# Performance work log

Hardware: AMD Instinct MI355X
Metric: run time of the kernel (lower is better)

Reference implementation:

```python
import jax, jax.numpy as jnp
import numpy as np

EMB = 1024
HEADS = 16
HEAD = EMB // HEADS
B, S = 4, 1024


def setup_inputs() -> dict:
    key = jax.random.key(0)
    ks = jax.random.split(key, 8)
    glorot = lambda k, shp: jax.random.normal(k, shp, jnp.float32) * np.sqrt(2.0 / (shp[-2] + shp[-1]))
    return {
        "inputs_for_keys": jax.random.normal(ks[0], (B, S, EMB), jnp.float32),
        "inputs_for_values": jax.random.normal(ks[1], (B, S, EMB), jnp.float32),
        "inputs_for_queries": jax.random.normal(ks[2], (B, S, EMB), jnp.float32),
        "Wk": glorot(ks[3], (HEADS, EMB, HEAD)),
        "Wv": glorot(ks[4], (HEADS, EMB, HEAD)),
        "Wq": glorot(ks[5], (HEADS, EMB, HEAD)),
        "Wo": glorot(ks[6], (EMB, EMB)),
        "bo": jnp.zeros((EMB,), jnp.float32),
    }


def reference(inputs_for_keys, inputs_for_values, inputs_for_queries, Wk, Wv, Wq, Wo, bo):
    # Batched equivalent of the per-head loop: project all heads at once.
    K = jnp.einsum("bse,hed->bhsd", inputs_for_keys, Wk)
    V = jnp.einsum("bse,hed->bhsd", inputs_for_values, Wv)
    Q = jnp.einsum("bse,hed->bhsd", inputs_for_queries, Wq)
    s_keys = K.shape[2]
    s_q = Q.shape[2]
    # causal mask: -inf strictly above diagonal (original: np.triu(ones*-inf, k=1))
    mask = jnp.where(jnp.triu(jnp.ones((s_q, s_keys), bool), k=1), -jnp.inf, 0.0).astype(jnp.float32)
    logits = jnp.einsum("bhqd,bhkd->bhqk", Q, K)
    # FAITHFUL quirk: original divides (logits + mask) by sqrt(window_size_keys)
    scores = jax.nn.softmax((logits + mask) / np.sqrt(s_keys), axis=-1)
    ctx = jnp.einsum("bhqk,bhkd->bhqd", scores, V)  # [B,H,Sq,Dh]
    # concat heads along last dim (head order matches loop order)
    concat = ctx.transpose(0, 2, 1, 3).reshape(ctx.shape[0], s_q, -1)  # [B,Sq,E]
    return jax.nn.relu(concat @ Wo + bo)
```

## Files before the change

### kernel.cpp

```cpp
#include <hip/hip_runtime.h>
#include <hip/hip_bf16.h>

typedef unsigned short u16;
typedef unsigned int   u32;
typedef __attribute__((ext_vector_type(4))) float f32x4;
typedef __attribute__((ext_vector_type(8))) short bf16x8;
typedef __attribute__((ext_vector_type(4))) short bf16x4;

#define EMB   1024
#define SEQ   1024
#define HEADS 16
#define DH    64
#define BATCH 4
#define BH    64
#define BS    4096
#define LDP   72
#define NEG_BIG (-1.0e30f)

__device__ __forceinline__ float b2f(u16 u){ return __uint_as_float(((u32)u) << 16); }
__device__ __forceinline__ u16 f2b(float f){
    u32 u = __float_as_uint(f);
    u32 r = u + 0x7fffu + ((u >> 16) & 1u);
    return (u16)(r >> 16);
}
__device__ __forceinline__ void zero4(f32x4& v){ v[0]=0.f; v[1]=0.f; v[2]=0.f; v[3]=0.f; }
__device__ __forceinline__ ushort4 pk4(float a, float b, float c, float d){
    ushort4 p; p.x = f2b(a); p.y = f2b(b); p.z = f2b(c); p.w = f2b(d); return p;
}

__device__ __forceinline__ void gld_lds16(const void* g, void* l){
    __builtin_amdgcn_global_load_lds(
        (const __attribute__((address_space(1))) u32*)g,
        (__attribute__((address_space(3))) u32*)l, 16, 0, 0);
}

__device__ __forceinline__ u16* tptr(u16* base, int row, int col ){
    const int phys = ((col >> 3) ^ (row & 7));
    return base + row * 64 + (phys << 3);
}
__device__ __forceinline__ const u16* tptrc(const u16* base, int row, int col ){
    const int phys = ((col >> 3) ^ (row & 7));
    return base + row * 64 + (phys << 3);
}
__device__ __forceinline__ const u16* tptr8c(const u16* base, int row, int col ){
    const int chunk = ((col >> 3) ^ (row & 7));
    return base + row * 64 + (chunk << 3) + (col & 7);
}

__device__ __forceinline__ void dot2_f32(const float* __restrict__ x,
                                         const float* __restrict__ w, const int ws,
                                         float& a0, float& a1)
{
    float s0 = 0.f, s1 = 0.f;
    for (int e = 0; e < EMB; e += 4) {
        const float4 xv = *(const float4*)(x + e);
        const float2 w0 = *(const float2*)(w + (size_t)(e + 0) * ws);
        const float2 w1 = *(const float2*)(w + (size_t)(e + 1) * ws);
        const float2 w2 = *(const float2*)(w + (size_t)(e + 2) * ws);
        const float2 w3 = *(const float2*)(w + (size_t)(e + 3) * ws);
        s0 += xv.x * w0.x; s1 += xv.x * w0.y;
        s0 += xv.y * w1.x; s1 += xv.y * w1.y;
        s0 += xv.z * w2.x; s1 += xv.z * w2.y;
        s0 += xv.w * w3.x; s1 += xv.w * w3.y;
    }
    a0 = s0; a1 = s1;
}


__global__ __launch_bounds__(256) void convert_x(
    const float* __restrict__ Xk, const float* __restrict__ Xv, const float* __restrict__ Xq,
    u16* __restrict__ XB)
{
    const int which = blockIdx.y;
    const float* __restrict__ src = (which == 0) ? Xk : (which == 1) ? Xv : Xq;
    const size_t off = (size_t)blockIdx.x * 1024 + threadIdx.x * 4;
    const float4 v = *(const float4*)(src + off);
    *(ushort4*)(XB + (size_t)which * 4194304 + off) = pk4(v.x, v.y, v.z, v.w);
}

__global__ __launch_bounds__(256) void transpose_w(
    const float* __restrict__ Wk, const float* __restrict__ Wv, const float* __restrict__ Wq,
    const float* __restrict__ Wo, u16* __restrict__ WT, u16* __restrict__ WoT)
{
    __shared__ u16 T[64][LDP];
    const int which = blockIdx.y;
    const int bx = blockIdx.x, t = threadIdx.x;

    if (which < 3) {
        const float* __restrict__ W = (which == 0) ? Wk : (which == 1) ? Wv : Wq;
        const int h = bx >> 4, e0 = (bx & 15) * 64;
        #pragma unroll
        for (int i = 0; i < 16; ++i) {
            const int idx = i * 256 + t;
            const int e = idx >> 6, d = idx & 63;
            T[d][e] = f2b(W[(size_t)h * (EMB * DH) + (size_t)(e0 + e) * DH + d]);
        }
        __syncthreads();
        u16* dstb = WT + (size_t)which * (EMB * EMB / 16) * 16;
        #pragma unroll
        for (int i = 0; i < 2; ++i) {
            const int idx = i * 256 + t;
            const int d = idx >> 3, e8 = (idx & 7) * 8;
            *(bf16x8*)(dstb + (size_t)(h * 64 + d) * EMB + e0 + e8) = *(const bf16x8*)&T[d][e8];
        }
    } else {
        const int j0 = (bx >> 4) * 64, e0 = (bx & 15) * 64;
        #pragma unroll
        for (int i = 0; i < 16; ++i) {
            const int idx = i * 256 + t;
            const int e = idx >> 6, d = idx & 63;
            T[d][e] = f2b(Wo[(size_t)(e0 + e) * EMB + j0 + d]);
        }
        __syncthreads();
        #pragma unroll
        for (int i = 0; i < 2; ++i) {
            const int idx = i * 256 + t;
            const int d = idx >> 3, e8 = (idx & 7) * 8;
            *(bf16x8*)(WoT + (size_t)(j0 + d) * EMB + e0 + e8) = *(const bf16x8*)&T[d][e8];
        }
    }
}

template<int MODE>
__global__ __launch_bounds__(256) void gemm128(
    const u16* __restrict__ XB, const u16* __restrict__ WT,
    u16* __restrict__ Qw, u16* __restrict__ Kw, u16* __restrict__ Vt,
    const float* __restrict__ bo, float* __restrict__ OUT)
{
    __shared__ u16 As[2][128 * 64];
    __shared__ u16 Bs[2][128 * 64];

    const int t = threadIdx.x;
    const int wave = t >> 6, lane = t & 63;
    const int quad = lane >> 4, l16 = lane & 15;
    const int wrow = wave >> 1, wcol = wave & 1;
    const int m0 = blockIdx.x * 128;
    const int n0 = blockIdx.y * 128;
    const int which = blockIdx.z;

    const u16* __restrict__ Ag = (MODE == 0) ? XB + (size_t)which * 4194304 : XB;
    const u16* __restrict__ Bg = (MODE == 0) ? WT + (size_t)which * 1048576 : WT;

    f32x4 acc[4][4];
    #pragma unroll
    for (int mi = 0; mi < 4; ++mi)
        #pragma unroll
        for (int ni = 0; ni < 4; ++ni) zero4(acc[mi][ni]);

    auto STAGE = [&](int kk, int buf){
        #pragma unroll
        for (int j = 0; j < 4; ++j) {
            const int cg = wave * 4 + j;
            const int c  = cg * 64 + lane;
            const int row = c >> 3;
            const int col = ((c ^ row) & 7) << 3;
            gld_lds16(Ag + (size_t)(m0 + row) * EMB + kk + col, &As[buf][cg * 512]);
            gld_lds16(Bg + (size_t)(n0 + row) * EMB + kk + col, &Bs[buf][cg * 512]);
        }
    };
    auto COMPUTE = [&](const u16* Ac, const u16* Bc){
        #pragma unroll
        for (int kb = 0; kb < 2; ++kb) {
            bf16x8 af[4], bf[4];
            #pragma unroll
            for (int mi = 0; mi < 4; ++mi)
                af[mi] = *(const bf16x8*)tptrc(Ac, wrow * 64 + mi * 16 + l16, kb * 32 + quad * 8);
            #pragma unroll
            for (int ni = 0; ni < 4; ++ni)
                bf[ni] = *(const bf16x8*)tptrc(Bc, wcol * 64 + ni * 16 + l16, kb * 32 + quad * 8);
            #pragma unroll
            for (int mi = 0; mi < 4; ++mi)
                #pragma unroll
                for (int ni = 0; ni < 4; ++ni)
                    acc[mi][ni] = __builtin_amdgcn_mfma_f32_16x16x32_bf16(af[mi], bf[ni], acc[mi][ni], 0, 0, 0);
        }
    };

    STAGE(0, 0);
    STAGE(64, 1);

    #pragma unroll
    for (int k = 0; k < 16; ++k) {
        if (k < 15) { asm volatile("s_waitcnt vmcnt(8)" ::: "memory"); }
        else        { asm volatile("s_waitcnt vmcnt(0)" ::: "memory"); }
        __builtin_amdgcn_sched_barrier(0);
        __builtin_amdgcn_s_barrier();
        __builtin_amdgcn_sched_barrier(0);

        COMPUTE(&As[k & 1][0], &Bs[k & 1][0]);

        asm volatile("s_waitcnt lgkmcnt(0)" ::: "memory");
        __builtin_amdgcn_sched_barrier(0);
        __builtin_amdgcn_s_barrier();
        __builtin_amdgcn_sched_barrier(0);

        if (k < 14) STAGE((k + 2) * 64, k & 1);
    }

    #pragma unroll
    for (int mi = 0; mi < 4; ++mi) {
        const int r = m0 + wrow * 64 + mi * 16 + quad * 4;
        #pragma unroll
        for (int ni = 0; ni < 4; ++ni) {
            const int j = n0 + wcol * 64 + ni * 16 + l16;
            if (MODE == 1) {
                const float bias = bo[j];
                #pragma unroll
                for (int reg = 0; reg < 4; ++reg) {
                    float v = acc[mi][ni][reg] + bias;
                    if (v < 0.f) v = 0.f;
                    OUT[(size_t)(r + reg) * EMB + j] = v;
                }
            } else {
                const int h = j >> 6, d = j & 63;
                const int b = r >> 10, s = r & (SEQ - 1);
                const int bh = b * HEADS + h;
                if (which == 1) {
                    *(ushort4*)(Vt + ((size_t)bh * DH + d) * SEQ + s) =
                        pk4(acc[mi][ni][0], acc[mi][ni][1], acc[mi][ni][2], acc[mi][ni][3]);
                } else {
                    u16* dst = (which == 0) ? Kw : Qw;
                    const float qsc = (which == 2) ? 0.03125f : 1.0f;
                    #pragma unroll
                    for (int reg = 0; reg < 4; ++reg)
                        dst[((size_t)bh * SEQ + s + reg) * DH + d] = f2b(acc[mi][ni][reg] * qsc);
                }
            }
        }
    }
}

__global__ __launch_bounds__(256) void attn_flash2(
    const u16* __restrict__ Qg, const u16* __restrict__ Kg, const u16* __restrict__ Vg,
    u16* __restrict__ CTXb)
{
    __shared__ u16 Ks[2][64 * 64];
    __shared__ u16 Vs[2][64 * 64];

    const int t = threadIdx.x;
    const int wave = t >> 6, lane = t & 63;
    const int quad = lane >> 4, l16 = lane & 15;
    const int bh = blockIdx.y;
    const int qt = (blockIdx.x + (blockIdx.y >> 2)) & 15;
    const int b = bh >> 4, h = bh & (HEADS - 1);
    const int q0 = qt * 64;

    const u16* __restrict__ Kbase = Kg + (size_t)bh * SEQ * DH;
    const u16* __restrict__ Vbase = Vg + (size_t)bh * DH * SEQ;

    bf16x8 qf[2];
    {
        const u16* qrow = Qg + ((size_t)bh * SEQ + q0 + wave * 16 + l16) * DH;
        qf[0] = *(const bf16x8*)(qrow + quad * 8);
        qf[1] = *(const bf16x8*)(qrow + 32 + quad * 8);
    }

    #pragma unroll
    for (int i = 0; i < 2; ++i) {
        const int c = i * 256 + t;
        const int row = c >> 3, col8 = (c & 7) * 8;
        const bf16x8 kv = *(const bf16x8*)(Kbase + (size_t)row * DH + col8);
        const bf16x8 vv = *(const bf16x8*)(Vbase + (size_t)row * SEQ + col8);
        *(bf16x8*)tptr(&Ks[0][0], row, col8) = kv;
        *(bf16x8*)tptr(&Vs[0][0], row, col8) = vv;
    }

    float m = NEG_BIG, l = 0.f;
    f32x4 oacc[4];
    #pragma unroll
    for (int nd = 0; nd < 4; ++nd) zero4(oacc[nd]);

    __syncthreads();

    const int qin = wave * 16 + l16;
    int cur = 0;
    for (int c = 0; c <= qt; ++c) {
        const int kn = ((c < qt) ? c + 1 : qt) * 64;
        bf16x8 kpre[2], vpre[2];
        #pragma unroll
        for (int i = 0; i < 2; ++i) {
            const int cc = i * 256 + t;
            const int row = cc >> 3, col8 = (cc & 7) * 8;
            kpre[i] = *(const bf16x8*)(Kbase + (size_t)(kn + row) * DH + col8);
            vpre[i] = *(const bf16x8*)(Vbase + (size_t)row * SEQ + kn + col8);
        }

        const u16* Kc = &Ks[cur][0];
        const u16* Vc = &Vs[cur][0];

        f32x4 sacc[4];
        #pragma unroll
        for (int ni = 0; ni < 4; ++ni) zero4(sacc[ni]);
        __builtin_amdgcn_s_setprio(1);
        #pragma unroll
        for (int kb = 0; kb < 2; ++kb) {
            #pragma unroll
            for (int ni = 0; ni < 4; ++ni) {
                const bf16x8 kf = *(const bf16x8*)tptrc(Kc, ni * 16 + l16, kb * 32 + quad * 8);
                sacc[ni] = __builtin_amdgcn_mfma_f32_16x16x32_bf16(kf, qf[kb], sacc[ni], 0, 0, 0);
            }
        }
        __builtin_amdgcn_s_setprio(0);

        const bool diag = (c == qt);
        float mx = m;
        #pragma unroll
        for (int ni = 0; ni < 4; ++ni) {
            #pragma unroll
            for (int reg = 0; reg < 4; ++reg) {
                float s = sacc[ni][reg];
                if (diag && (ni * 16 + quad * 4 + reg > qin)) s = NEG_BIG;
                sacc[ni][reg] = s;
                mx = fmaxf(mx, s);
            }
        }
        mx = fmaxf(mx, __shfl_xor(mx, 16));
        mx = fmaxf(mx, __shfl_xor(mx, 32));
        const float alpha = __expf(m - mx);
        m = mx;
        float rs = 0.f;
        bf16x4 pa[4];
        #pragma unroll
        for (int ni = 0; ni < 4; ++ni) {
            const float p0 = __expf(sacc[ni][0] - mx);
            const float p1 = __expf(sacc[ni][1] - mx);
            const float p2 = __expf(sacc[ni][2] - mx);
            const float p3 = __expf(sacc[ni][3] - mx);
            rs += (p0 + p1) + (p2 + p3);
            bf16x4 pk;
            pk[0] = (short)f2b(p0); pk[1] = (short)f2b(p1);
            pk[2] = (short)f2b(p2); pk[3] = (short)f2b(p3);
            pa[ni] = pk;
        }
        rs += __shfl_xor(rs, 16);
        rs += __shfl_xor(rs, 32);
        l = l * alpha + rs;

        #pragma unroll
        for (int reg = 0; reg < 4; ++reg) {
            const float ar = __shfl(alpha, quad * 4 + reg);
            #pragma unroll
            for (int nd = 0; nd < 4; ++nd) oacc[nd][reg] *= ar;
        }

        __builtin_amdgcn_s_setprio(1);
        #pragma unroll
        for (int ks = 0; ks < 4; ++ks) {
            #pragma unroll
            for (int nd = 0; nd < 4; ++nd) {
                const bf16x4 vf = *(const bf16x4*)tptr8c(Vc, nd * 16 + l16, ks * 16 + quad * 4);
                oacc[nd] = __builtin_amdgcn_mfma_f32_16x16x16bf16_1k(pa[ks], vf, oacc[nd], 0, 0, 0);
            }
        }
        __builtin_amdgcn_s_setprio(0);

        const int nxt = cur ^ 1;
        #pragma unroll
        for (int i = 0; i < 2; ++i) {
            const int cc = i * 256 + t;
            const int row = cc >> 3, col8 = (cc & 7) * 8;
            *(bf16x8*)tptr(&Ks[nxt][0], row, col8) = kpre[i];
            *(bf16x8*)tptr(&Vs[nxt][0], row, col8) = vpre[i];
        }
        __syncthreads();
        cur = nxt;
    }

    #pragma unroll
    for (int reg = 0; reg < 4; ++reg) {
        const float il = 1.f / __shfl(l, quad * 4 + reg);
        const int q = q0 + wave * 16 + quad * 4 + reg;
        #pragma unroll
        for (int nd = 0; nd < 4; ++nd) {
            const int d = nd * 16 + l16;
            CTXb[(size_t)(b * SEQ + q) * EMB + h * DH + d] = f2b(oacc[nd][reg] * il);
        }
    }
}


__global__ __launch_bounds__(256) void qkv_proj_mfma(
    const float* __restrict__ Xk, const float* __restrict__ Xv, const float* __restrict__ Xq,
    const float* __restrict__ Wk, const float* __restrict__ Wv, const float* __restrict__ Wq,
    u16* __restrict__ Kw, u16* __restrict__ Vw, u16* __restrict__ Qw)
{
    __shared__ u16 As[128][LDP];
    __shared__ u16 Bs[64][LDP];

    const int which = blockIdx.z;
    const float* __restrict__ X = (which == 0) ? Xk : (which == 1) ? Xv : Xq;
    const float* __restrict__ W = (which == 0) ? Wk : (which == 1) ? Wv : Wq;

    const int h    = blockIdx.y;
    const int m0   = blockIdx.x * 128;
    const int t    = threadIdx.x;
    const int wave = t >> 6, lane = t & 63;
    const int quad = lane >> 4, l16 = lane & 15;

    f32x4 acc[2][4];
    #pragma unroll
    for (int mi = 0; mi < 2; ++mi)
        #pragma unroll
        for (int ni = 0; ni < 4; ++ni) zero4(acc[mi][ni]);

    const size_t wbase = (size_t)h * EMB * DH;
    for (int k0 = 0; k0 < EMB; k0 += 64) {
        #pragma unroll
        for (int i = 0; i < 8; ++i) {
            const int idx = i * 256 + t;
            const int r = idx >> 4, c4 = (idx & 15) * 4;
            const float4 v = *(const float4*)(X + (size_t)(m0 + r) * EMB + k0 + c4);
            *(ushort4*)&As[r][c4] = pk4(v.x, v.y, v.z, v.w);
        }
        #pragma unroll
        for (int i = 0; i < 4; ++i) {
            const int d  = t & 63;
            const int e0 = (t >> 6) * 4 + i * 16;
            const float v0 = W[wbase + (size_t)(k0 + e0 + 0) * DH + d];
            const float v1 = W[wbase + (size_t)(k0 + e0 + 1) * DH + d];
            const float v2 = W[wbase + (size_t)(k0 + e0 + 2) * DH + d];
            const float v3 = W[wbase + (size_t)(k0 + e0 + 3) * DH + d];
            *(ushort4*)&Bs[d][e0] = pk4(v0, v1, v2, v3);
        }
        __syncthreads();

        #pragma unroll
        for (int kb = 0; kb < 2; ++kb) {
            bf16x8 bfr[4];
            #pragma unroll
            for (int ni = 0; ni < 4; ++ni)
                bfr[ni] = *(const bf16x8*)&Bs[ni * 16 + l16][kb * 32 + quad * 8];
            #pragma unroll
            for (int mi = 0; mi < 2; ++mi) {
                const bf16x8 af = *(const bf16x8*)&As[wave * 32 + mi * 16 + l16][kb * 32 + quad * 8];
                #pragma unroll
                for (int ni = 0; ni < 4; ++ni)
                    acc[mi][ni] = __builtin_amdgcn_mfma_f32_16x16x32_bf16(af, bfr[ni], acc[mi][ni], 0, 0, 0);
            }
        }
        __syncthreads();
    }

    const int b  = m0 >> 10;
    const int bh = b * HEADS + h;
    u16* __restrict__ RowDst = (which == 0) ? Kw : Qw;
    #pragma unroll
    for (int mi = 0; mi < 2; ++mi) {
        const int s_base = (m0 & (SEQ - 1)) + wave * 32 + mi * 16 + quad * 4;
        #pragma unroll
        for (int ni = 0; ni < 4; ++ni) {
            const int d = ni * 16 + l16;
            if (which != 1) {
                #pragma unroll
                for (int reg = 0; reg < 4; ++reg)
                    RowDst[((size_t)bh * SEQ + s_base + reg) * DH + d] = f2b(acc[mi][ni][reg]);
            } else {
                *(ushort4*)(Vw + ((size_t)bh * DH + d) * SEQ + s_base) =
                    pk4(acc[mi][ni][0], acc[mi][ni][1], acc[mi][ni][2], acc[mi][ni][3]);
            }
        }
    }
}

template<bool QWS, bool TOWS>
__global__ __launch_bounds__(256) void attn_flash(
    const float* __restrict__ Xq, const float* __restrict__ Wq,
    const u16* __restrict__ Qg, const u16* __restrict__ Kg, const u16* __restrict__ Vg,
    u16* __restrict__ CTXb, float* __restrict__ CTXf)
{
    __shared__ u16 Qs[64][LDP];
    union KVU {
        struct { u16 Ks[64][LDP]; u16 Vt[64][LDP]; } kv;
        struct { u16 Xs[64][LDP]; u16 WT[64][LDP]; } pr;
    };
    __shared__ KVU uu;
    __shared__ u16 Ps[64][LDP];

    const int t    = threadIdx.x;
    const int wave = t >> 6, lane = t & 63;
    const int quad = lane >> 4, l16 = lane & 15;
    const int qt = blockIdx.x, bh = blockIdx.y;
    const int b  = bh >> 4, h = bh & (HEADS - 1);
    const int q0 = qt * 64;

    if (QWS) {
        #pragma unroll
        for (int i = 0; i < 4; ++i) {
            const int idx = i * 256 + t;
            const int r = idx >> 4, c4 = (idx & 15) * 4;
            *(ushort4*)&Qs[r][c4] = *(const ushort4*)(Qg + ((size_t)bh * SEQ + q0 + r) * DH + c4);
        }
    } else {
        f32x4 qacc[4];
        #pragma unroll
        for (int ni = 0; ni < 4; ++ni) zero4(qacc[ni]);
        const size_t wbase = (size_t)h * EMB * DH;
        for (int k0 = 0; k0 < EMB; k0 += 64) {
            #pragma unroll
            for (int i = 0; i < 4; ++i) {
                const int idx = i * 256 + t;
                const int r = idx >> 4, c4 = (idx & 15) * 4;
                const float4 v = *(const float4*)(Xq + (size_t)(b * SEQ + q0 + r) * EMB + k0 + c4);
                *(ushort4*)&uu.pr.Xs[r][c4] = pk4(v.x, v.y, v.z, v.w);
            }
            #pragma unroll
            for (int i = 0; i < 4; ++i) {
                const int d  = t & 63;
                const int e0 = (t >> 6) * 4 + i * 16;
                const float v0 = Wq[wbase + (size_t)(k0 + e0 + 0) * DH + d];
                const float v1 = Wq[wbase + (size_t)(k0 + e0 + 1) * DH + d];
                const float v2 = Wq[wbase + (size_t)(k0 + e0 + 2) * DH + d];
                const float v3 = Wq[wbase + (size_t)(k0 + e0 + 3) * DH + d];
                *(ushort4*)&uu.pr.WT[d][e0] = pk4(v0, v1, v2, v3);
            }
            __syncthreads();
            #pragma unroll
            for (int kb = 0; kb < 2; ++kb) {
                const bf16x8 af = *(const bf16x8*)&uu.pr.Xs[wave * 16 + l16][kb * 32 + quad * 8];
                #pragma unroll
                for (int ni = 0; ni < 4; ++ni) {
                    const bf16x8 bf = *(const bf16x8*)&uu.pr.WT[ni * 16 + l16][kb * 32 + quad * 8];
                    qacc[ni] = __builtin_amdgcn_mfma_f32_16x16x32_bf16(af, bf, qacc[ni], 0, 0, 0);
                }
            }
            __syncthreads();
        }
        #pragma unroll
        for (int ni = 0; ni < 4; ++ni)
            #pragma unroll
            for (int reg = 0; reg < 4; ++reg)
                Qs[wave * 16 + quad * 4 + reg][ni * 16 + l16] = f2b(qacc[ni][reg]);
    }

    float m[4], l[4];
    #pragma unroll
    for (int reg = 0; reg < 4; ++reg) { m[reg] = NEG_BIG; l[reg] = 0.f; }
    f32x4 oacc[4];
    #pragma unroll
    for (int ni = 0; ni < 4; ++ni) zero4(oacc[ni]);
    __syncthreads();

    for (int c = 0; c <= qt; ++c) {
        const int k0 = c * 64;

        #pragma unroll
        for (int i = 0; i < 4; ++i) {
            const int idx = i * 256 + t;
            const int r = idx >> 4, c4 = (idx & 15) * 4;
            *(ushort4*)&uu.kv.Ks[r][c4] = *(const ushort4*)(Kg + ((size_t)bh * SEQ + k0 + r) * DH + c4);
        }
        #pragma unroll
        for (int i = 0; i < 4; ++i) {
            const int idx = i * 256 + t;
            const int r = idx >> 4, c4 = (idx & 15) * 4;
            *(ushort4*)&uu.kv.Vt[r][c4] = *(const ushort4*)(Vg + ((size_t)bh * DH + r) * SEQ + k0 + c4);
        }
        __syncthreads();

        f32x4 sacc[4];
        #pragma unroll
        for (int ni = 0; ni < 4; ++ni) zero4(sacc[ni]);
        #pragma unroll
        for (int kb = 0; kb < 2; ++kb) {
            const bf16x8 af = *(const bf16x8*)&Qs[wave * 16 + l16][kb * 32 + quad * 8];
            #pragma unroll
            for (int ni = 0; ni < 4; ++ni) {
                const bf16x8 bf = *(const bf16x8*)&uu.kv.Ks[ni * 16 + l16][kb * 32 + quad * 8];
                sacc[ni] = __builtin_amdgcn_mfma_f32_16x16x32_bf16(af, bf, sacc[ni], 0, 0, 0);
            }
        }

        const bool diag = (c == qt);
        #pragma unroll
        for (int reg = 0; reg < 4; ++reg) {
            const int rloc = quad * 4 + reg;
            float sv[4];
            #pragma unroll
            for (int ni = 0; ni < 4; ++ni) {
                float s = sacc[ni][reg] * 0.03125f;
                if (diag && (ni * 16 + l16 > wave * 16 + rloc)) s = NEG_BIG;
                sv[ni] = s;
            }
            float mx = fmaxf(fmaxf(sv[0], sv[1]), fmaxf(sv[2], sv[3]));
            mx = fmaxf(mx, m[reg]);
            #pragma unroll
            for (int off = 1; off < 16; off <<= 1) mx = fmaxf(mx, __shfl_xor(mx, off));
            const float alpha = __expf(m[reg] - mx);
            float rs = 0.f;
            #pragma unroll
            for (int ni = 0; ni < 4; ++ni) {
                const float p = __expf(sv[ni] - mx);
                Ps[wave * 16 + rloc][ni * 16 + l16] = f2b(p);
                rs += p;
            }
            #pragma unroll
            for (int off = 1; off < 16; off <<= 1) rs += __shfl_xor(rs, off);
            l[reg] = l[reg] * alpha + rs;
            m[reg] = mx;
            #pragma unroll
            for (int ni = 0; ni < 4; ++ni) oacc[ni][reg] *= alpha;
        }
        __syncthreads();

        #pragma unroll
        for (int kb = 0; kb < 2; ++kb) {
            const bf16x8 af = *(const bf16x8*)&Ps[wave * 16 + l16][kb * 32 + quad * 8];
            #pragma unroll
            for (int ni = 0; ni < 4; ++ni) {
                const bf16x8 bf = *(const bf16x8*)&uu.kv.Vt[ni * 16 + l16][kb * 32 + quad * 8];
                oacc[ni] = __builtin_amdgcn_mfma_f32_16x16x32_bf16(af, bf, oacc[ni], 0, 0, 0);
            }
        }
        __syncthreads();
    }

    float il[4];
    #pragma unroll
    for (int reg = 0; reg < 4; ++reg) il[reg] = 1.f / l[reg];
    #pragma unroll
    for (int ni = 0; ni < 4; ++ni) {
        const int d = ni * 16 + l16;
        #pragma unroll
        for (int reg = 0; reg < 4; ++reg) {
            const int q = wave * 16 + quad * 4 + reg;
            const float val = oacc[ni][reg] * il[reg];
            const size_t off = ((size_t)(b * SEQ + q0 + q)) * EMB + h * DH + d;
            if (TOWS) CTXb[off] = f2b(val);
            else      CTXf[off] = val;
        }
    }
}

__global__ __launch_bounds__(256) void out_proj_mfma(
    const u16* __restrict__ CTXb, const float* __restrict__ Wo,
    const float* __restrict__ bo, float* __restrict__ OUT)
{
    __shared__ u16 As[128][LDP];
    __shared__ u16 Bs[64][LDP];

    const int m0 = blockIdx.x * 128;
    const int n0 = blockIdx.y * 64;
    const int t = threadIdx.x;
    const int wave = t >> 6, lane = t & 63;
    const int quad = lane >> 4, l16 = lane & 15;

    f32x4 acc[2][4];
    #pragma unroll
    for (int mi = 0; mi < 2; ++mi)
        #pragma unroll
        for (int ni = 0; ni < 4; ++ni) zero4(acc[mi][ni]);

    for (int k0 = 0; k0 < EMB; k0 += 64) {
        #pragma unroll
        for (int i = 0; i < 8; ++i) {
            const int idx = i * 256 + t;
            const int r = idx >> 4, c4 = (idx & 15) * 4;
            *(ushort4*)&As[r][c4] = *(const ushort4*)(CTXb + (size_t)(m0 + r) * EMB + k0 + c4);
        }
        #pragma unroll
        for (int i = 0; i < 4; ++i) {
            const int d  = t & 63;
            const int e0 = (t >> 6) * 4 + i * 16;
            const float v0 = Wo[(size_t)(k0 + e0 + 0) * EMB + n0 + d];
            const float v1 = Wo[(size_t)(k0 + e0 + 1) * EMB + n0 + d];
            const float v2 = Wo[(size_t)(k0 + e0 + 2) * EMB + n0 + d];
            const float v3 = Wo[(size_t)(k0 + e0 + 3) * EMB + n0 + d];
            *(ushort4*)&Bs[d][e0] = pk4(v0, v1, v2, v3);
        }
        __syncthreads();
        #pragma unroll
        for (int kb = 0; kb < 2; ++kb) {
            bf16x8 bfr[4];
            #pragma unroll
            for (int ni = 0; ni < 4; ++ni)
                bfr[ni] = *(const bf16x8*)&Bs[ni * 16 + l16][kb * 32 + quad * 8];
            #pragma unroll
            for (int mi = 0; mi < 2; ++mi) {
                const bf16x8 af = *(const bf16x8*)&As[wave * 32 + mi * 16 + l16][kb * 32 + quad * 8];
                #pragma unroll
                for (int ni = 0; ni < 4; ++ni)
                    acc[mi][ni] = __builtin_amdgcn_mfma_f32_16x16x32_bf16(af, bfr[ni], acc[mi][ni], 0, 0, 0);
            }
        }
        __syncthreads();
    }

    #pragma unroll
    for (int mi = 0; mi < 2; ++mi) {
        const int row = m0 + wave * 32 + mi * 16 + quad * 4;
        #pragma unroll
        for (int ni = 0; ni < 4; ++ni) {
            const int col = n0 + ni * 16 + l16;
            const float bias = bo[col];
            #pragma unroll
            for (int reg = 0; reg < 4; ++reg) {
                float v = acc[mi][ni][reg] + bias;
                if (v < 0.f) v = 0.f;
                OUT[(size_t)(row + reg) * EMB + col] = v;
            }
        }
    }
}

__global__ __launch_bounds__(256) void out_proj_inplace(
    float* __restrict__ OUT, const float* __restrict__ Wo, const float* __restrict__ bo)
{
    __shared__ float Xs[8][EMB];
    const int t    = threadIdx.x;
    const int row0 = blockIdx.x * 8;
    {
        const float4* src = (const float4*)(OUT + (size_t)row0 * EMB);
        float4* dst = (float4*)&Xs[0][0];
        #pragma unroll
        for (int i = 0; i < 8; ++i) dst[i * 256 + t] = src[i * 256 + t];
    }
    __syncthreads();
    const int r  = t >> 5;
    const int j0 = (t & 31) * 2;
    const float* xrow = Xs[r];
    for (int jb = 0; jb < 16; ++jb) {
        const int j = jb * 64 + j0;
        float a0, a1;
        dot2_f32(xrow, Wo + j, EMB, a0, a1);
        a0 += bo[j];     if (a0 < 0.f) a0 = 0.f;
        a1 += bo[j + 1]; if (a1 < 0.f) a1 = 0.f;
        float* op = OUT + (size_t)(row0 + r) * EMB + j;
        op[0] = a0; op[1] = a1;
    }
}

extern "C" void kernel_launch(void* const* d_in, const int* in_sizes, int n_in,
                              void* d_out, int out_size, void* d_ws, size_t ws_size,
                              hipStream_t stream)
{
    const float* Xk = (const float*)d_in[0];
    const float* Xv = (const float*)d_in[1];
    const float* Xq = (const float*)d_in[2];
    const float* Wk = (const float*)d_in[3];
    const float* Wv = (const float*)d_in[4];
    const float* Wq = (const float*)d_in[5];
    const float* Wo = (const float*)d_in[6];
    const float* bo = (const float*)d_in[7];
    float* OUT = (float*)d_out;
    (void)in_sizes; (void)n_in; (void)out_size;

    const size_t SEGE = (size_t)BH * SEQ * DH;
    const size_t SEGB = SEGE * sizeof(u16);

    const size_t XB_OFF  = 0;
    const size_t WT_OFF  = 3 * SEGE;
    const size_t WOT_OFF = WT_OFF + 3 * (EMB * EMB / 64) * 64;
    const size_t QW_OFF  = WOT_OFF + (size_t)EMB * EMB;
    const size_t KW_OFF  = QW_OFF + SEGE;
    const size_t VT_OFF  = KW_OFF + SEGE;
    const size_t TIER_A_BYTES = (VT_OFF + SEGE) * sizeof(u16);

    if (ws_size >= TIER_A_BYTES) {
        u16* W16 = (u16*)d_ws;
        u16* XB  = W16 + XB_OFF;
        u16* WT  = W16 + WT_OFF;
        u16* WoT = W16 + WOT_OFF;
        u16* Qw  = W16 + QW_OFF;
        u16* Kw  = W16 + KW_OFF;
        u16* Vt  = W16 + VT_OFF;
        u16* CTX = XB;

        convert_x<<<dim3(4096, 3), 256, 0, stream>>>(Xk, Xv, Xq, XB);
        transpose_w<<<dim3(256, 4), 256, 0, stream>>>(Wk, Wv, Wq, Wo, WT, WoT);
        gemm128<0><<<dim3(32, 8, 3), 256, 0, stream>>>(XB, WT, Qw, Kw, Vt, nullptr, nullptr);
        attn_flash2<<<dim3(SEQ / 64, BH), 256, 0, stream>>>(Qw, Kw, Vt, CTX);
        gemm128<1><<<dim3(32, 8, 1), 256, 0, stream>>>(CTX, WoT, nullptr, nullptr, nullptr, bo, OUT);
    } else if (ws_size >= 4 * SEGB) {
        u16* Qw = (u16*)d_ws;
        u16* Kw = Qw + SEGE;
        u16* Vw = Kw + SEGE;
        u16* CT = Vw + SEGE;
        qkv_proj_mfma<<<dim3(32, HEADS, 3), 256, 0, stream>>>(Xk, Xv, Xq, Wk, Wv, Wq, Kw, Vw, Qw);
        attn_flash<true, true><<<dim3(SEQ / 64, BH), 256, 0, stream>>>(
            Xq, Wq, Qw, Kw, Vw, CT, nullptr);
        out_proj_mfma<<<dim3(32, EMB / 64), 256, 0, stream>>>(CT, Wo, bo, OUT);
    } else if (ws_size >= 3 * SEGB) {
        u16* Kw = (u16*)d_ws;
        u16* Vw = Kw + SEGE;
        u16* CT = Vw + SEGE;
        qkv_proj_mfma<<<dim3(32, HEADS, 2), 256, 0, stream>>>(Xk, Xv, Xq, Wk, Wv, Wq, Kw, Vw, nullptr);
        attn_flash<false, true><<<dim3(SEQ / 64, BH), 256, 0, stream>>>(
            Xq, Wq, nullptr, Kw, Vw, CT, nullptr);
        out_proj_mfma<<<dim3(32, EMB / 64), 256, 0, stream>>>(CT, Wo, bo, OUT);
    } else {
        u16* Kw = (u16*)d_ws;
        u16* Vw = Kw + SEGE;
        qkv_proj_mfma<<<dim3(32, HEADS, 2), 256, 0, stream>>>(Xk, Xv, Xq, Wk, Wv, Wq, Kw, Vw, nullptr);
        attn_flash<false, false><<<dim3(SEQ / 64, BH), 256, 0, stream>>>(
            Xq, Wq, nullptr, Kw, Vw, nullptr, OUT);
        out_proj_inplace<<<dim3(BS / 8), 256, 0, stream>>>(OUT, Wo, bo);
    }
}
```

Before: 204.8 us.

## Use exp2 softmax with lazy rescaling and packed bf16 conversion

Folds log2(e) into the Q scaling so the attention softmax can use the native exp2 instruction instead of __expf. Adds a wave-uniform threshold test so the running max and the O-accumulator rescale happen only when the tile max exceeds the stored max by more than 11 (in log2 units). Replaces the software bf16 rounding of probabilities with the hardware v_cvt_pk_bf16_f32 instruction. This trims VALU work in the softmax inner loop, at the cost of probabilities up to 2^11 before normalization, which adds some overflow and precision risk in bf16/fp32.

After: 199.6 us. 1.03x faster.

```diff
diff --git a/kernel.cpp b/kernel.cpp
--- a/kernel.cpp
+++ b/kernel.cpp
@@ -27,6 +27,7 @@
 __device__ __forceinline__ ushort4 pk4(float a, float b, float c, float d){
     ushort4 p; p.x = f2b(a); p.y = f2b(b); p.z = f2b(c); p.w = f2b(d); return p;
 }
+__device__ __forceinline__ float exp2g(float x){ return __builtin_amdgcn_exp2f(x); }
 
 __device__ __forceinline__ void gld_lds16(const void* g, void* l){
     __builtin_amdgcn_global_load_lds(
@@ -220,7 +221,7 @@
                         pk4(acc[mi][ni][0], acc[mi][ni][1], acc[mi][ni][2], acc[mi][ni][3]);
                 } else {
                     u16* dst = (which == 0) ? Kw : Qw;
-                    const float qsc = (which == 2) ? 0.03125f : 1.0f;
+                    const float qsc = (which == 2) ? 0.03125f * 1.44269504088896f : 1.0f;
                     #pragma unroll
                     for (int reg = 0; reg < 4; ++reg)
                         dst[((size_t)bh * SEQ + s + reg) * DH + d] = f2b(acc[mi][ni][reg] * qsc);
@@ -303,7 +304,7 @@
         __builtin_amdgcn_s_setprio(0);
 
         const bool diag = (c == qt);
-        float mx = m;
+        float tmx[4];
         #pragma unroll
         for (int ni = 0; ni < 4; ++ni) {
             #pragma unroll
@@ -311,37 +312,44 @@
                 float s = sacc[ni][reg];
                 if (diag && (ni * 16 + quad * 4 + reg > qin)) s = NEG_BIG;
                 sacc[ni][reg] = s;
-                mx = fmaxf(mx, s);
-            }
-        }
-        mx = fmaxf(mx, __shfl_xor(mx, 16));
-        mx = fmaxf(mx, __shfl_xor(mx, 32));
-        const float alpha = __expf(m - mx);
-        m = mx;
+            }
+            tmx[ni] = fmaxf(fmaxf(sacc[ni][0], sacc[ni][1]),
+                            fmaxf(sacc[ni][2], sacc[ni][3]));
+        }
+        float pmax = fmaxf(fmaxf(tmx[0], tmx[1]), fmaxf(tmx[2], tmx[3]));
+        pmax = fmaxf(pmax, __shfl_xor(pmax, 16));
+        pmax = fmaxf(pmax, __shfl_xor(pmax, 32));
+
+        if (!__all((int)(pmax - m <= 11.0f))) {
+            const float mx = fmaxf(m, pmax);
+            const float alpha = exp2g(m - mx);
+            m = mx;
+            l *= alpha;
+            #pragma unroll
+            for (int reg = 0; reg < 4; ++reg) {
+                const float ar = __shfl(alpha, quad * 4 + reg);
+                #pragma unroll
+                for (int nd = 0; nd < 4; ++nd) oacc[nd][reg] *= ar;
+            }
+        }
+
         float rs = 0.f;
         bf16x4 pa[4];
         #pragma unroll
         for (int ni = 0; ni < 4; ++ni) {
-            const float p0 = __expf(sacc[ni][0] - mx);
-            const float p1 = __expf(sacc[ni][1] - mx);
-            const float p2 = __expf(sacc[ni][2] - mx);
-            const float p3 = __expf(sacc[ni][3] - mx);
+            const float p0 = exp2g(sacc[ni][0] - m);
+            const float p1 = exp2g(sacc[ni][1] - m);
+            const float p2 = exp2g(sacc[ni][2] - m);
+            const float p3 = exp2g(sacc[ni][3] - m);
             rs += (p0 + p1) + (p2 + p3);
-            bf16x4 pk;
-            pk[0] = (short)f2b(p0); pk[1] = (short)f2b(p1);
-            pk[2] = (short)f2b(p2); pk[3] = (short)f2b(p3);
-            pa[ni] = pk;
+            union { bf16x4 v; u32 d[2]; } pk;
+            asm("v_cvt_pk_bf16_f32 %0, %1, %2" : "=v"(pk.d[0]) : "v"(p0), "v"(p1));
+            asm("v_cvt_pk_bf16_f32 %0, %1, %2" : "=v"(pk.d[1]) : "v"(p2), "v"(p3));
+            pa[ni] = pk.v;
         }
         rs += __shfl_xor(rs, 16);
         rs += __shfl_xor(rs, 32);
-        l = l * alpha + rs;
-
-        #pragma unroll
-        for (int reg = 0; reg < 4; ++reg) {
-            const float ar = __shfl(alpha, quad * 4 + reg);
-            #pragma unroll
-            for (int nd = 0; nd < 4; ++nd) oacc[nd][reg] *= ar;
-        }
+        l += rs;
 
         __builtin_amdgcn_s_setprio(1);
         #pragma unroll
```
